# Kernel optimization log

Measured on AMD Instinct MI355X. Metric: run time of the kernel, lower is better.

The kernel has to match this reference:

```python
import jax, jax.numpy as jnp
import numpy as np

_SAMPLING_EPS = 1e-5
_NEG_INF = -jnp.inf


def _apply_min_p(logits, min_p):
    # probs >= min_p * max_prob are kept (vLLM apply_min_p)
    probs = jax.nn.softmax(logits, axis=-1)
    max_p = jnp.max(probs, axis=-1, keepdims=True)
    keep = probs >= (min_p[:, None] * max_p)
    return jnp.where(keep, logits, _NEG_INF)


def _apply_top_k_top_p(logits, top_k, top_p):
    # One descending sort serves both filters (mirrors vLLM topk/topp kernel).
    T, V = logits.shape
    sorted_l = jnp.sort(logits, axis=-1)[:, ::-1]  # [T, V] descending
    # top-k threshold: k-th largest logit; top_k <= 0 means disabled
    k = jnp.where(top_k <= 0, V, jnp.clip(top_k, 1, V)).astype(jnp.int32)
    kth = jnp.take_along_axis(sorted_l, (k - 1)[:, None], axis=-1)  # [T, 1]
    # top-p: keep smallest prefix whose prob mass reaches top_p (first token always kept)
    probs = jax.nn.softmax(sorted_l, axis=-1)
    cum = jnp.cumsum(probs, axis=-1)
    keep_p = (cum - probs) < top_p[:, None]
    pth = jnp.min(jnp.where(keep_p, sorted_l, jnp.inf), axis=-1, keepdims=True)
    keep = (logits >= kth) & (logits >= pth)
    return jnp.where(keep, logits, _NEG_INF)


def _gather_logprobs(logprobs, num_logprobs, token_ids):
    # vLLM gather_logprobs: topk + sampled-token logprob + rank
    topk_lp, topk_idx = jax.lax.top_k(logprobs, num_logprobs)  # [T, K]
    tok = token_ids[:, None]  # [T, 1]
    tok_lp = jnp.take_along_axis(logprobs, tok, axis=-1)  # [T, 1]
    ranks = jnp.sum(logprobs >= tok_lp, axis=-1).astype(jnp.int32)  # [T]
    indices = jnp.concatenate([tok, topk_idx], axis=1).astype(jnp.int32)
    lps = jnp.concatenate([tok_lp, topk_lp], axis=1)
    return indices, lps, ranks


def setup_inputs() -> dict:
    key = jax.random.key(0)
    k1, k2, k3, k4, k5, k6 = jax.random.split(key, 6)
    T, V = 256, 128256
    logits = jax.random.normal(k1, (T, V), dtype=jnp.float32)
    temperature = 0.2 + 1.3 * jax.random.uniform(k2, (T,), dtype=jnp.float32)
    # every 8th request is greedy (temperature < _SAMPLING_EPS path)
    temperature = jnp.where(jnp.arange(T) % 8 == 0, 0.0, temperature)
    min_p = 0.05 * jax.random.uniform(k3, (T,), dtype=jnp.float32)
    top_p = 0.5 + 0.5 * jax.random.uniform(k4, (T,), dtype=jnp.float32)
    top_k = jax.random.randint(k5, (T,), 0, 64, dtype=jnp.int32)
    u = jax.random.uniform(k6, (T, V), dtype=jnp.float32, minval=1e-10, maxval=1.0)
    return {"logits": logits, "temperature": temperature, "min_p": min_p,
            "top_p": top_p, "top_k": top_k, "u": u, "num_logprobs": 20}


def reference(logits, temperature, min_p, top_p, top_k, u, num_logprobs):
    logits = logits.astype(jnp.float32)
    # logprobs computed on raw (pre-temperature) logits, as in vLLM
    raw_logprobs = jax.nn.log_softmax(logits, axis=-1)
    # greedy path
    greedy = jnp.argmax(logits, axis=-1)
    # random path: temperature -> min_p -> top-k/top-p -> gumbel-max sample
    is_greedy = temperature < _SAMPLING_EPS
    safe_temp = jnp.where(is_greedy, 1.0, temperature)  # rows with temp<eps use greedy anyway
    l = logits / safe_temp[:, None]
    l = _apply_min_p(l, min_p)
    l = _apply_top_k_top_p(l, top_k, top_p)
    gumbel = -jnp.log(-jnp.log(u))  # u in (0,1)
    random_sampled = jnp.argmax(l + gumbel, axis=-1)
    sampled = jnp.where(is_greedy, greedy, random_sampled)
    indices, lps, ranks = _gather_logprobs(raw_logprobs, num_logprobs, sampled)
    sampled_token_ids = sampled.astype(jnp.int32)[:, None]  # [T, 1]
    return sampled_token_ids, indices, lps, ranks
```

## Files before the change

### kernel.cpp

```cpp
#include <hip/hip_runtime.h>
#include <math.h>

#define TPB 1024
#define TPBS 256
#define NS 8
#define NBINS 512
#define CAP 2048
#define NSEL 64
#define MBINS 1024
#define MWIN 16.0f
#define WIN 2.0f
#define SLCAP 1024
#define BANDCAP 64

typedef unsigned long long u64t;

__device__ __forceinline__ unsigned int ordAsc(float v) {
  unsigned int b = __float_as_uint(v);
  return (b & 0x80000000u) ? ~b : (b | 0x80000000u);
}
__device__ __forceinline__ float ordInv(unsigned int o) {
  return __uint_as_float((o & 0x80000000u) ? (o & 0x7fffffffu) : ~o);
}
__device__ __forceinline__ unsigned int fkeyDesc(float v) { return ~ordAsc(v); }
__device__ __forceinline__ float fkeyInv(unsigned int kd) { return ordInv(~kd); }
__device__ __forceinline__ u64t mkMaxKey(float v, int idx) {
  return ((u64t)ordAsc(v) << 32) | (unsigned int)(~(unsigned int)idx);
}

__device__ __forceinline__ float blockSumF(float v, float* sred) {
  #pragma unroll
  for (int o = 32; o > 0; o >>= 1) v += __shfl_down(v, o, 64);
  int wid = threadIdx.x >> 6, lane = threadIdx.x & 63, nw = blockDim.x >> 6;
  __syncthreads();
  if (lane == 0) sred[wid] = v;
  __syncthreads();
  if (threadIdx.x == 0) { float r = sred[0]; for (int w = 1; w < nw; ++w) r += sred[w]; sred[0] = r; }
  __syncthreads();
  float r = sred[0];
  __syncthreads();
  return r;
}
__device__ __forceinline__ int blockSumI(int v, int* sred) {
  #pragma unroll
  for (int o = 32; o > 0; o >>= 1) v += __shfl_down(v, o, 64);
  int wid = threadIdx.x >> 6, lane = threadIdx.x & 63, nw = blockDim.x >> 6;
  __syncthreads();
  if (lane == 0) sred[wid] = v;
  __syncthreads();
  if (threadIdx.x == 0) { int r = sred[0]; for (int w = 1; w < nw; ++w) r += sred[w]; sred[0] = r; }
  __syncthreads();
  int r = sred[0];
  __syncthreads();
  return r;
}
__device__ __forceinline__ int blockMaxI(int v, int* sred) {
  #pragma unroll
  for (int o = 32; o > 0; o >>= 1) { int v2 = __shfl_down(v, o, 64); if (v2 > v) v = v2; }
  int wid = threadIdx.x >> 6, lane = threadIdx.x & 63, nw = blockDim.x >> 6;
  __syncthreads();
  if (lane == 0) sred[wid] = v;
  __syncthreads();
  if (threadIdx.x == 0) { int r = sred[0]; for (int w = 1; w < nw; ++w) if (sred[w] > r) r = sred[w]; sred[0] = r; }
  __syncthreads();
  int r = sred[0];
  __syncthreads();
  return r;
}
__device__ __forceinline__ u64t blockMaxU64(u64t v, u64t* sred) {
  #pragma unroll
  for (int o = 32; o > 0; o >>= 1) { u64t v2 = __shfl_down(v, o, 64); if (v2 > v) v = v2; }
  int wid = threadIdx.x >> 6, lane = threadIdx.x & 63, nw = blockDim.x >> 6;
  __syncthreads();
  if (lane == 0) sred[wid] = v;
  __syncthreads();
  if (threadIdx.x == 0) { u64t r = sred[0]; for (int w = 1; w < nw; ++w) if (sred[w] > r) r = sred[w]; sred[0] = r; }
  __syncthreads();
  u64t r = sred[0];
  __syncthreads();
  return r;
}
__device__ __forceinline__ void blockArgMaxF(float& v, int& idx, float* sredf, int* sredi) {
  #pragma unroll
  for (int o = 32; o > 0; o >>= 1) {
    float v2 = __shfl_down(v, o, 64);
    int  i2 = __shfl_down(idx, o, 64);
    if (v2 > v || (v2 == v && i2 < idx)) { v = v2; idx = i2; }
  }
  int wid = threadIdx.x >> 6, lane = threadIdx.x & 63, nw = blockDim.x >> 6;
  __syncthreads();
  if (lane == 0) { sredf[wid] = v; sredi[wid] = idx; }
  __syncthreads();
  if (threadIdx.x == 0) {
    float bv = sredf[0]; int bi = sredi[0];
    for (int w = 1; w < nw; ++w) {
      float v2 = sredf[w]; int i2 = sredi[w];
      if (v2 > bv || (v2 == bv && i2 < bi)) { bv = v2; bi = i2; }
    }
    sredf[0] = bv; sredi[0] = bi;
  }
  __syncthreads();
  v = sredf[0]; idx = sredi[0];
  __syncthreads();
}

__device__ void bitonicSortN(u64t* keys, int n) {
  for (unsigned int k = 2; k <= (unsigned int)n; k <<= 1) {
    for (unsigned int j = k >> 1; j > 0; j >>= 1) {
      __syncthreads();
      for (unsigned int i = threadIdx.x; i < (unsigned int)n; i += blockDim.x) {
        unsigned int ixj = i ^ j;
        if (ixj > i) {
          u64t a = keys[i], b = keys[ixj];
          bool up = ((i & k) == 0);
          if ((a > b) == up) { keys[i] = b; keys[ixj] = a; }
        }
      }
    }
  }
  __syncthreads();
}

__device__ u64t bitonicReg1024(u64t key, u64t* lds) {
  const int tid = threadIdx.x;
  for (unsigned int k = 2; k <= 1024; k <<= 1) {
    for (unsigned int j = k >> 1; j > 0; j >>= 1) {
      u64t partner;
      if (j >= 64) {
        __syncthreads();
        lds[tid] = key;
        __syncthreads();
        partner = lds[tid ^ j];
      } else {
        partner = __shfl_xor((unsigned long long)key, (int)j, 64);
      }
      bool up = ((tid & k) == 0);
      bool lower = ((tid & j) == 0);
      bool keepSmaller = (up == lower);
      bool pSmaller = (partner < key);
      if (keepSmaller == pSmaller) key = partner;
    }
  }
  __syncthreads();
  lds[tid] = key;
  __syncthreads();
  return key;
}

__device__ __forceinline__ float combineS0(const u64t* smax, const float* s0s, float m0) {
  float S0 = 0.f;
  for (int w = 0; w < NS; ++w) {
    float ms = ordInv((unsigned int)(smax[w] >> 32));
    S0 += s0s[w] * expf(ms - m0);
  }
  return S0;
}

__global__ __launch_bounds__(TPBS) void k1_max(const float* __restrict__ logits,
                                               u64t* __restrict__ maxes,
                                               float* __restrict__ s0_ws,
                                               int* __restrict__ ccnt,
                                               int* __restrict__ bandcnt, int V) {
  const int row = blockIdx.y, s = blockIdx.x, tid = threadIdx.x;
  if (s == 0 && tid == 0) { ccnt[row] = 0; bandcnt[row] = 0; }
  const float* x = logits + (size_t)row * V;
  const int V4 = V >> 2;
  const float4* x4 = (const float4*)x;
  const int a4 = (int)(((long long)V4 * s) / NS), b4 = (int)(((long long)V4 * (s + 1)) / NS);
  u64t best = 0ull;
  float mt = -INFINITY, s0 = 0.f;
  auto body = [&](float vv, int gi) {
    u64t k = mkMaxKey(vv, gi);
    if (k > best) best = k;
    if (vv > mt) { s0 = s0 * expf(mt - vv); mt = vv; }
    s0 += expf(vv - mt);
  };
  for (int i4 = a4 + tid; i4 < b4; i4 += TPBS) {
    float4 v = x4[i4]; int b = i4 << 2;
    body(v.x, b); body(v.y, b + 1); body(v.z, b + 2); body(v.w, b + 3);
  }
  if (s == NS - 1) for (int i = (V4 << 2) + tid; i < V; i += TPBS) body(x[i], i);
  __shared__ u64t sredU[16];
  __shared__ float sredF[16];
  best = blockMaxU64(best, sredU);
  if (tid == 0) maxes[row * NS + s] = best;
  const float msv = ordInv((unsigned int)(best >> 32));
  float s0r = s0 * expf(mt - msv);
  float r0 = blockSumF(s0r, sredF);
  if (tid == 0) s0_ws[row * NS + s] = r0;
}

__global__ __launch_bounds__(TPBS) void k2_all(const float* __restrict__ logits,
    const float* __restrict__ temp_arr, const float* __restrict__ minp_arr,
    const int* __restrict__ topk_arr, const u64t* __restrict__ maxes,
    float* __restrict__ sl_ws, float* __restrict__ sp_ws, int* __restrict__ ck_ws,
    int* __restrict__ ccnt, u64t* __restrict__ cand,
    int* __restrict__ bandcnt, u64t* __restrict__ band,
    u64t* __restrict__ mass, int V) {
  const int row = blockIdx.y, s = blockIdx.x, tid = threadIdx.x;
  __shared__ u64t smax[NS];
  __shared__ float sredF[16];
  __shared__ int sredI[16];
  __shared__ u64t lcand[SLCAP];
  __shared__ u64t lmass[MBINS];
  __shared__ int lcnt, lbase;
  const float temp = temp_arr[row];
  const bool greedy = (temp < 1e-5f);
  const int topk = topk_arr[row];
  const bool deep = (!greedy && topk <= 0);
  if (tid < NS) smax[tid] = maxes[row * NS + tid];
  if (tid == 0) lcnt = 0;
  if (deep) for (int b = tid; b < MBINS; b += TPBS) lmass[b] = 0ull;
  __syncthreads();
  u64t mk = smax[0];
  for (int w = 1; w < NS; ++w) { u64t t = smax[w]; if (t > mk) mk = t; }
  const float m0 = ordInv((unsigned int)(mk >> 32));
  const float wlo = m0 - WIN;
  const float* x = logits + (size_t)row * V;
  const int V4 = V >> 2;
  const float4* x4 = (const float4*)x;
  const int a4 = (int)(((long long)V4 * s) / NS), b4 = (int)(((long long)V4 * (s + 1)) / NS);

  if (greedy) {
    auto bodyG = [&](float vv, int gi) {
      if (vv >= wlo) {
        int pos = atomicAdd(&lcnt, 1);
        if (pos < SLCAP) lcand[pos] = ((u64t)fkeyDesc(vv) << 32) | (unsigned int)gi;
      }
    };
    for (int i4 = a4 + tid; i4 < b4; i4 += TPBS) {
      float4 v = x4[i4]; int b = i4 << 2;
      bodyG(v.x, b); bodyG(v.y, b + 1); bodyG(v.z, b + 2); bodyG(v.w, b + 3);
    }
    if (s == NS - 1) for (int i = (V4 << 2) + tid; i < V; i += TPBS) bodyG(x[i], i);
    __syncthreads();
    if (tid == 0) {
      sl_ws[row * NS + s] = 0.f; sp_ws[row * NS + s] = 0.f; ck_ws[row * NS + s] = 0;
      int c = lcnt;
      int add = (c > SLCAP) ? (c + CAP + 1) : c;
      lbase = atomicAdd(&ccnt[row], add);
    }
    __syncthreads();
    int c = lcnt < SLCAP ? lcnt : SLCAP;
    int base = lbase;
    for (int j = tid; j < c; j += TPBS) {
      int pos = base + j;
      if (pos < CAP) cand[(size_t)row * CAP + pos] = lcand[j];
    }
    return;
  }

  const float st = temp;
  const float ml = m0 / st;
  const float minp = minp_arr[row];
  const float bHi = minp * (1.0f + 4e-6f);
  const float bLo = minp * (1.0f - 4e-6f);
  const float scaleM = (float)MBINS / MWIN;
  float sl = 0.f, sp = 0.f; int ckp = 0;
  auto body = [&](float vv, int gi) {
    float l = vv / st;
    float e = expf(l - ml);
    sl += e;
    if (minp <= 0.f || e > bHi) {
      sp += e; ckp++;
      if (deep) {
        float fm = (m0 - vv) * scaleM;
        if (fm < (float)MBINS)
          atomicAdd(&lmass[(int)fm], (u64t)((double)e * 4294967296.0));
      }
    } else if (e >= bLo) {
      int pos = atomicAdd(&bandcnt[row], 1);
      if (pos < BANDCAP)
        band[(size_t)row * BANDCAP + pos] = ((u64t)(unsigned int)gi << 32) | __float_as_uint(vv);
    }
    if (vv >= wlo) {
      int pos = atomicAdd(&lcnt, 1);
      if (pos < SLCAP) lcand[pos] = ((u64t)fkeyDesc(vv) << 32) | (unsigned int)gi;
    }
  };
  for (int i4 = a4 + tid; i4 < b4; i4 += TPBS) {
    float4 v = x4[i4]; int b = i4 << 2;
    body(v.x, b); body(v.y, b + 1); body(v.z, b + 2); body(v.w, b + 3);
  }
  if (s == NS - 1) for (int i = (V4 << 2) + tid; i < V; i += TPBS) body(x[i], i);
  float rl = blockSumF(sl, sredF);
  float rp = blockSumF(sp, sredF);
  int rc = blockSumI(ckp, sredI);
  if (tid == 0) {
    sl_ws[row * NS + s] = rl; sp_ws[row * NS + s] = rp; ck_ws[row * NS + s] = rc;
    int c = lcnt;
    int add = (c > SLCAP) ? (c + CAP + 1) : c;
    lbase = atomicAdd(&ccnt[row], add);
  }
  __syncthreads();
  int c = lcnt < SLCAP ? lcnt : SLCAP;
  int base = lbase;
  for (int j = tid; j < c; j += TPBS) {
    int pos = base + j;
    if (pos < CAP) cand[(size_t)row * CAP + pos] = lcand[j];
  }
  if (deep) {
    u64t* mrow = mass + ((size_t)row * NS + s) * MBINS;
    for (int b = tid; b < MBINS; b += TPBS) mrow[b] = lmass[b];
  }
}

__global__ __launch_bounds__(TPB) void k5_final(const float* __restrict__ logits,
    const float* __restrict__ temp_arr, const float* __restrict__ minp_arr,
    const float* __restrict__ topp_arr, const int* __restrict__ topk_arr,
    const float* __restrict__ u_arr, const u64t* __restrict__ maxes,
    const float* __restrict__ s0_ws, const float* __restrict__ sl_ws,
    const float* __restrict__ sp_ws, const int* __restrict__ ck_ws,
    const int* __restrict__ ccnt, const u64t* __restrict__ cand,
    const u64t* __restrict__ mass, const u64t* __restrict__ band,
    const int* __restrict__ bandcnt, float* __restrict__ w_thr,
    int* __restrict__ w_bpM, double* __restrict__ w_seed, float* __restrict__ w_spD,
    float* __restrict__ out, int T, int V, int NL) {
  __shared__ u64t keyA[CAP];
  __shared__ int fh[NBINS];
  __shared__ float sredF[16];
  __shared__ int sredI[16];
  __shared__ u64t smax[NS];
  __shared__ float sp0[NS], spl[NS], spsp[NS];
  __shared__ int spck[NS];
  __shared__ float sh_thresh, sh_toklp, sh_spAdd;
  __shared__ double sh_seed;
  __shared__ int sh_cnt, sh_bp, sh_bCnt, sh_ckAdd;
  __shared__ u64t sh_bKeys[BANDCAP];
  __shared__ u64t sh_bMass[BANDCAP];
  __shared__ int  sh_bBin[BANDCAP];
  __shared__ u64t kb64[NSEL];
  __shared__ u64t kbs[NSEL];

  const int row = blockIdx.x;
  const int tid = threadIdx.x;
  const float* x  = logits + (size_t)row * V;
  const float* uu = u_arr  + (size_t)row * V;
  const float temp = temp_arr[row];
  const float minp = minp_arr[row];
  const float topp = topp_arr[row];
  const int   topk = topk_arr[row];
  const bool greedy = (temp < 1e-5f);
  const float st = greedy ? 1.0f : temp;
  const int V4 = V >> 2;
  const float4* x4 = (const float4*)x;

  if (tid < NS) {
    smax[tid] = maxes[row * NS + tid];
    sp0[tid] = s0_ws[row * NS + tid];
    spl[tid] = sl_ws[row * NS + tid];
    spsp[tid] = sp_ws[row * NS + tid];
    spck[tid] = ck_ws[row * NS + tid];
  }
  __syncthreads();
  u64t mk = smax[0];
  for (int w = 1; w < NS; ++w) { u64t t = smax[w]; if (t > mk) mk = t; }
  const float m0 = ordInv((unsigned int)(mk >> 32));
  const int gidx = (int)(~(unsigned int)mk);
  float S = spl[0], Sp = spsp[0];
  int ck = spck[0];
  for (int w = 1; w < NS; ++w) { S += spl[w]; Sp += spsp[w]; ck += spck[w]; }
  const float S0 = combineS0(smax, sp0, m0);
  const float ml = m0 / st;
  const float logS0 = logf(S0);
  const float rhs = minp * (1.0f / S);
  const float rhsS = rhs * S;
  const float rhsHi = rhsS * (1.0f + 1e-6f);
  const float rhsLo = rhsS * (1.0f - 1e-6f);
  auto keepTest = [&](float e) -> bool {
    if (e > rhsHi) return true;
    if (e < rhsLo) return false;
    return (e / S) >= rhs;
  };
  const bool deep = (!greedy && topk <= 0);
  const float scaleM = (float)MBINS / MWIN;

  const int bandTotal = greedy ? 0 : bandcnt[row];
  const bool bandOv = bandTotal > BANDCAP;
  if (tid == 0) { sh_bCnt = 0; sh_spAdd = 0.f; sh_ckAdd = 0; }
  __syncthreads();
  if (!greedy && !bandOv && bandTotal > 0 && minp > 0.f) {
    if (tid == 0) {
      for (int i = 0; i < bandTotal; ++i) sh_bKeys[i] = band[(size_t)row * BANDCAP + i];
      for (int i = 1; i < bandTotal; ++i) {
        u64t k = sh_bKeys[i]; int j = i - 1;
        while (j >= 0 && sh_bKeys[j] > k) { sh_bKeys[j + 1] = sh_bKeys[j]; j--; }
        sh_bKeys[j + 1] = k;
      }
      float spAdd = 0.f; int ckAdd = 0, bc = 0;
      for (int i = 0; i < bandTotal; ++i) {
        float vv = __uint_as_float((unsigned int)(sh_bKeys[i] & 0xffffffffu));
        float l = vv / st; float e = expf(l - ml);
        if ((e / S) >= rhs) {
          spAdd += e; ckAdd++;
          if (deep) {
            float fm = (m0 - vv) * scaleM;
            if (fm < (float)MBINS) { sh_bBin[bc] = (int)fm; sh_bMass[bc] = (u64t)((double)e * 4294967296.0); bc++; }
          }
        }
      }
      sh_spAdd = spAdd; sh_ckAdd = ckAdd; sh_bCnt = bc;
    }
    __syncthreads();
    Sp += sh_spAdd; ck += sh_ckAdd;
  } else if (!greedy && bandOv) {
    float sp2 = 0.f; int ck2 = 0;
    auto bodyR = [&](float vv) {
      float l = vv / st; float e = expf(l - ml);
      if (keepTest(e)) { sp2 += e; ck2++; }
    };
    for (int i4 = tid; i4 < V4; i4 += TPB) { float4 v = x4[i4]; bodyR(v.x); bodyR(v.y); bodyR(v.z); bodyR(v.w); }
    for (int i = (V4 << 2) + tid; i < V; i += TPB) bodyR(x[i]);
    Sp = blockSumF(sp2, sredF);
    ck = blockSumI(ck2, sredI);
  }

  int cc = ccnt[row];
  int Cact = cc < CAP ? cc : CAP;
  int need = NSEL;
  if (topk > need) need = topk;
  if (need > CAP / 2) need = CAP / 2;
  if (need > V) need = V;
  bool fb = (cc > CAP) || (Cact < need);
  if (!fb) {
    for (int j = tid; j < Cact; j += TPB) keyA[j] = cand[(size_t)row * CAP + j];
  } else {
    const float bS = (float)NBINS / MWIN;
    for (int b = tid; b < NBINS; b += TPB) fh[b] = 0;
    if (tid == 0) sh_cnt = 0;
    __syncthreads();
    auto hb = [&](float vv) {
      float fbv = (m0 - vv) * bS;
      if (fbv < (float)NBINS) atomicAdd(&fh[(int)fbv], 1);
    };
    for (int i4 = tid; i4 < V4; i4 += TPB) { float4 v = x4[i4]; hb(v.x); hb(v.y); hb(v.z); hb(v.w); }
    for (int i = (V4 << 2) + tid; i < V; i += TPB) hb(x[i]);
    __syncthreads();
    if (tid == 0) {
      int cum = 0, B = -1;
      for (int b = 0; b < NBINS; ++b) { cum += fh[b]; if (cum >= need) { B = b; break; } }
      if (B < 0) B = NBINS - 1;
      sh_bp = B;
    }
    __syncthreads();
    const int B = sh_bp;
    auto cb = [&](float vv, int gi) {
      float fbv = (m0 - vv) * bS;
      if (fbv < (float)NBINS && (int)fbv <= B) {
        int pos = atomicAdd(&sh_cnt, 1);
        if (pos < CAP) keyA[pos] = ((u64t)fkeyDesc(vv) << 32) | (unsigned int)gi;
      }
    };
    for (int i4 = tid; i4 < V4; i4 += TPB) { float4 v = x4[i4]; int b = i4 << 2; cb(v.x, b); cb(v.y, b + 1); cb(v.z, b + 2); cb(v.w, b + 3); }
    for (int i = (V4 << 2) + tid; i < V; i += TPB) cb(x[i], i);
    __syncthreads();
    Cact = sh_cnt < CAP ? sh_cnt : CAP;
  }
  __syncthreads();
  if (Cact <= 1024) {
    u64t ka = (tid < Cact) ? keyA[tid] : ~0ull;
    bitonicReg1024(ka, keyA);
  } else {
    int n = 128; while (n < Cact) n <<= 1;
    for (int i = Cact + tid; i < n; i += TPB) keyA[i] = ~0ull;
    __syncthreads();
    bitonicSortN(keyA, n);
  }
  {
    int M = Cact < NSEL ? Cact : NSEL;
    if (tid < M) {
      u64t ka = keyA[tid];
      float xv = fkeyInv((unsigned int)(ka >> 32));
      float lp = (xv - m0) - logS0;
      kb64[tid] = ((u64t)fkeyDesc(lp) << 32) | (ka & 0xffffffffu);
    }
    __syncthreads();
    if (tid < M) {
      u64t me = kb64[tid];
      int r = 0;
      for (int i = 0; i < M; ++i) r += (kb64[i] < me) ? 1 : 0;
      kbs[r] = me;
    }
    __syncthreads();
    float* o_idx  = out + T;
    float* o_lps  = out + T + (size_t)T * (NL + 1);
    for (int j = tid; j < NL; j += TPB) {
      if (j < M) {
        u64t kb = kbs[j];
        o_idx[(size_t)row * (NL + 1) + 1 + j] = (float)(unsigned int)(kb & 0xffffffffu);
        o_lps[(size_t)row * (NL + 1) + 1 + j] = fkeyInv((unsigned int)(kb >> 32));
      }
    }
  }

  int sampled = -1;
  if (greedy) {
    sampled = gidx;
  } else if (topk > 0) {
    if (tid == 0) {
      int k = topk; if (k > V) k = V; if (k > CAP) k = CAP;
      int jp = 0; float cum = 0.f;
      for (int j = 0; j < k; ++j) {
        float pj = 0.f;
        if (j < ck && j < Cact) {
          float xv = fkeyInv((unsigned int)(keyA[j] >> 32));
          pj = expf(xv / st - ml) / Sp;
        }
        cum += pj;
        float ex = cum - pj;
        if (ex < topp) jp = j;
      }
      float thr;
      if (jp < ck && jp < Cact) {
        float xv = fkeyInv((unsigned int)(keyA[jp] >> 32));
        thr = xv / st;
      } else thr = -INFINITY;
      sh_thresh = thr;
    }
    __syncthreads();
    const float thr = sh_thresh;
    float bm = -INFINITY; int bi = 0x7fffffff;
    for (int j = tid; j < Cact; j += TPB) {
      u64t ka = keyA[j];
      float xv = fkeyInv((unsigned int)(ka >> 32));
      int gi = (int)(ka & 0xffffffffu);
      float l = xv / st;
      float e = expf(l - ml);
      if (keepTest(e) && l >= thr) {
        float uv = uu[gi];
        float g = -logf(-logf(uv));
        float val = l + g;
        if (val > bm || (val == bm && gi < bi)) { bm = val; bi = gi; }
      }
    }
    blockArgMaxF(bm, bi, sredF, sredI);
    sampled = bi;
  } else {
    if (!bandOv) {
      if (tid < MBINS) {
        u64t m = 0;
        for (int w = 0; w < NS; ++w) m += mass[((size_t)row * NS + w) * MBINS + tid];
        int bc = sh_bCnt;
        for (int j = 0; j < bc; ++j) if (sh_bBin[j] == tid) m += sh_bMass[j];
        keyA[tid] = m;
      }
    } else {
      for (int b = tid; b < MBINS; b += TPB) keyA[b] = 0ull;
      __syncthreads();
      auto bodyM = [&](float vv) {
        float l = vv / st; float e = expf(l - ml);
        if (keepTest(e)) {
          float fm = (m0 - vv) * scaleM;
          if (fm < (float)MBINS) atomicAdd(&keyA[(int)fm], (u64t)((double)e * 4294967296.0));
        }
      };
      for (int i4 = tid; i4 < V4; i4 += TPB) { float4 v = x4[i4]; bodyM(v.x); bodyM(v.y); bodyM(v.z); bodyM(v.w); }
      for (int i = (V4 << 2) + tid; i < V; i += TPB) bodyM(x[i]);
    }
    __syncthreads();
    u64t mh = (tid < MBINS) ? keyA[tid] : 0ull;
    for (int off = 1; off < MBINS; off <<= 1) {
      u64t add = (tid < MBINS && tid >= off) ? keyA[tid - off] : 0ull;
      __syncthreads();
      if (tid < MBINS) keyA[tid] += add;
      __syncthreads();
    }
    const double TP = (double)topp * (double)Sp;
    int q = -1; u64t myexcl = 0;
    if (tid < MBINS && mh > 0ull) {
      u64t excl = keyA[tid] - mh;
      if ((double)excl * (1.0 / 4294967296.0) < TP) { q = tid; myexcl = excl; }
    }
    int bp = blockMaxI(q, sredI);
    if (bp >= 0 && tid == bp) sh_seed = (double)myexcl * (1.0 / 4294967296.0);
    if (bp < 0 && tid == 0) sh_seed = 0.0;
    __syncthreads();
    if (tid == 0) {
      w_bpM[row] = bp;
      w_seed[row] = sh_seed;
      w_spD[row] = Sp;
      if (bp < 0) w_thr[row] = -INFINITY;
    }
  }

  if (!deep) {
    if (tid == 0) sh_toklp = (x[sampled] - m0) - logS0;
    __syncthreads();
    const float toklp = sh_toklp;
    int rc = 0;
    for (int j = tid; j < Cact; j += TPB) {
      float xv = fkeyInv((unsigned int)(keyA[j] >> 32));
      float lp = (xv - m0) - logS0;
      if (lp >= toklp) rc++;
    }
    int rank = blockSumI(rc, sredI);
    float* o_samp = out;
    float* o_idx  = out + T;
    float* o_lps  = out + T + (size_t)T * (NL + 1);
    float* o_rank = out + T + (size_t)2 * T * (NL + 1);
    if (tid == 0) {
      o_samp[row] = (float)sampled;
      o_idx[(size_t)row * (NL + 1)] = (float)sampled;
      o_lps[(size_t)row * (NL + 1)] = toklp;
      o_rank[row] = (float)rank;
    }
  }
}

__global__ __launch_bounds__(TPB) void kD_thr(const float* __restrict__ logits,
    const float* __restrict__ temp_arr, const float* __restrict__ minp_arr,
    const float* __restrict__ topp_arr, const int* __restrict__ topk_arr,
    const u64t* __restrict__ maxes, const float* __restrict__ sl_ws,
    const int* __restrict__ w_bpM, const float* __restrict__ w_spD,
    const double* __restrict__ w_seed, float* __restrict__ w_thr, int V) {
  const int row = blockIdx.x, tid = threadIdx.x;
  const float temp = temp_arr[row];
  if (temp < 1e-5f || topk_arr[row] > 0) return;
  const int bp = w_bpM[row];
  if (bp < 0) return;
  __shared__ u64t keyA[CAP];
  __shared__ float pvals[CAP];
  __shared__ u64t smax[NS];
  __shared__ float ssl[NS];
  __shared__ int sh_cnt;
  if (tid < NS) { smax[tid] = maxes[row * NS + tid]; ssl[tid] = sl_ws[row * NS + tid]; }
  if (tid == 0) sh_cnt = 0;
  __syncthreads();
  u64t mk = smax[0];
  for (int w = 1; w < NS; ++w) { u64t t = smax[w]; if (t > mk) mk = t; }
  float S = ssl[0];
  for (int w = 1; w < NS; ++w) S += ssl[w];
  const float m0 = ordInv((unsigned int)(mk >> 32));
  const float st = temp;
  const float ml = m0 / st;
  const float minp = minp_arr[row];
  const float rhs = minp * (1.0f / S);
  const float rhsS = rhs * S;
  const float rhsHi = rhsS * (1.0f + 1e-6f);
  const float rhsLo = rhsS * (1.0f - 1e-6f);
  auto keepTest = [&](float e) -> bool {
    if (e > rhsHi) return true;
    if (e < rhsLo) return false;
    return (e / S) >= rhs;
  };
  const float scaleM = (float)MBINS / MWIN;
  const float* x = logits + (size_t)row * V;
  const int V4 = V >> 2;
  const float4* x4 = (const float4*)x;
  auto body = [&](float vv, int gi) {
    float fm = (m0 - vv) * scaleM;
    if (fm < (float)MBINS && (int)fm == bp) {
      float l = vv / st;
      float e = expf(l - ml);
      if (keepTest(e)) {
        int pos = atomicAdd(&sh_cnt, 1);
        if (pos < CAP) keyA[pos] = ((u64t)fkeyDesc(vv) << 32) | (unsigned int)gi;
      }
    }
  };
  for (int i4 = tid; i4 < V4; i4 += TPB) {
    float4 v = x4[i4]; int b = i4 << 2;
    body(v.x, b); body(v.y, b + 1); body(v.z, b + 2); body(v.w, b + 3);
  }
  for (int i = (V4 << 2) + tid; i < V; i += TPB) body(x[i], i);
  __syncthreads();
  int C5 = sh_cnt < CAP ? sh_cnt : CAP;
  if (C5 <= 1024) {
    u64t kc = (tid < C5) ? keyA[tid] : ~0ull;
    bitonicReg1024(kc, keyA);
  } else {
    int n5 = 128; while (n5 < C5) n5 <<= 1;
    for (int i = C5 + tid; i < n5; i += TPB) keyA[i] = ~0ull;
    __syncthreads();
    bitonicSortN(keyA, n5);
  }
  const float Sp = w_spD[row];
  for (int j = tid; j < C5; j += TPB) {
    float xv = fkeyInv((unsigned int)(keyA[j] >> 32));
    pvals[j] = expf(xv / st - ml) / Sp;
  }
  __syncthreads();
  if (tid == 0) {
    const float topp = topp_arr[row];
    float cum = (float)(w_seed[row] / (double)Sp);
    float lastVal = fkeyInv((unsigned int)(keyA[0] >> 32));
    for (int j = 0; j < C5; ++j) {
      float pj = pvals[j];
      cum += pj;
      float ex = cum - pj;
      if (ex < topp) lastVal = fkeyInv((unsigned int)(keyA[j] >> 32));
    }
    w_thr[row] = lastVal / st;
  }
}

__global__ __launch_bounds__(TPBS) void k6_gumbel(const float* __restrict__ logits,
    const float* __restrict__ temp_arr, const float* __restrict__ minp_arr,
    const int* __restrict__ topk_arr, const float* __restrict__ u_arr,
    const u64t* __restrict__ maxes, const float* __restrict__ sl_ws,
    const float* __restrict__ w_thr, u64t* __restrict__ gkey, int V) {
  const int row = blockIdx.y, s = blockIdx.x, tid = threadIdx.x;
  const float temp = temp_arr[row];
  if (temp < 1e-5f || topk_arr[row] > 0) return;
  __shared__ u64t smax[NS];
  __shared__ float ssl[NS];
  __shared__ float sredF[16];
  __shared__ int sredI[16];
  if (tid < NS) { smax[tid] = maxes[row * NS + tid]; ssl[tid] = sl_ws[row * NS + tid]; }
  __syncthreads();
  u64t mk = smax[0];
  for (int w = 1; w < NS; ++w) { u64t t = smax[w]; if (t > mk) mk = t; }
  float S = ssl[0];
  for (int w = 1; w < NS; ++w) S += ssl[w];
  const float m0 = ordInv((unsigned int)(mk >> 32));
  const float st = temp;
  const float ml = m0 / st;
  const float minp = minp_arr[row];
  const float rhs = minp * (1.0f / S);
  const float rhsS = rhs * S;
  const float rhsHi = rhsS * (1.0f + 1e-6f);
  const float rhsLo = rhsS * (1.0f - 1e-6f);
  auto keepTest = [&](float e) -> bool {
    if (e > rhsHi) return true;
    if (e < rhsLo) return false;
    return (e / S) >= rhs;
  };
  const float thr = w_thr[row];
  const float* x  = logits + (size_t)row * V;
  const float* uu = u_arr  + (size_t)row * V;
  const int V4 = V >> 2;
  const float4* x4 = (const float4*)x;
  const float4* u4 = (const float4*)uu;
  const int a4 = (int)(((long long)V4 * s) / NS), b4 = (int)(((long long)V4 * (s + 1)) / NS);
  float bm = -INFINITY; int bi = 0x7fffffff;
  auto body = [&](float vv, float uv, int gi) {
    float l = vv / st;
    float e = expf(l - ml);
    if (keepTest(e) && l >= thr) {
      float g = -logf(-logf(uv));
      float val = l + g;
      if (val > bm || (val == bm && gi < bi)) { bm = val; bi = gi; }
    }
  };
  for (int i4 = a4 + tid; i4 < b4; i4 += TPBS) {
    float4 v = x4[i4]; float4 w = u4[i4]; int b = i4 << 2;
    body(v.x, w.x, b); body(v.y, w.y, b + 1); body(v.z, w.z, b + 2); body(v.w, w.w, b + 3);
  }
  if (s == NS - 1) for (int i = (V4 << 2) + tid; i < V; i += TPBS) body(x[i], uu[i], i);
  blockArgMaxF(bm, bi, sredF, sredI);
  if (tid == 0) gkey[row * NS + s] = mkMaxKey(bm, bi);
}

__global__ __launch_bounds__(TPB) void k7_deepfin(const float* __restrict__ logits,
    const float* __restrict__ temp_arr, const int* __restrict__ topk_arr,
    const u64t* __restrict__ gkey, const float* __restrict__ s0_ws,
    const u64t* __restrict__ maxes, float* __restrict__ out, int T, int V, int NL) {
  const int row = blockIdx.x, tid = threadIdx.x;
  const float temp = temp_arr[row];
  if (temp < 1e-5f || topk_arr[row] > 0) return;
  __shared__ u64t sg[NS];
  __shared__ u64t smax[NS];
  __shared__ float sp0[NS];
  __shared__ int sredI[16];
  if (tid < NS) { sg[tid] = gkey[row * NS + tid]; smax[tid] = maxes[row * NS + tid]; sp0[tid] = s0_ws[row * NS + tid]; }
  __syncthreads();
  u64t gk = sg[0];
  for (int w = 1; w < NS; ++w) { if (sg[w] > gk) gk = sg[w]; }
  u64t mk = smax[0];
  for (int w = 1; w < NS; ++w) { u64t t = smax[w]; if (t > mk) mk = t; }
  const float m0 = ordInv((unsigned int)(mk >> 32));
  const float S0 = combineS0(smax, sp0, m0);
  const float logS0 = logf(S0);
  const int sampled = (int)(~(unsigned int)gk);
  const float* x = logits + (size_t)row * V;
  const float toklp = (x[sampled] - m0) - logS0;
  const int V4 = V >> 2;
  const float4* x4 = (const float4*)x;
  int rc = 0;
  auto body = [&](float vv) {
    float lp = (vv - m0) - logS0;
    if (lp >= toklp) rc++;
  };
  for (int i4 = tid; i4 < V4; i4 += TPB) { float4 v = x4[i4]; body(v.x); body(v.y); body(v.z); body(v.w); }
  for (int i = (V4 << 2) + tid; i < V; i += TPB) body(x[i]);
  int rank = blockSumI(rc, sredI);
  float* o_samp = out;
  float* o_idx  = out + T;
  float* o_lps  = out + T + (size_t)T * (NL + 1);
  float* o_rank = out + T + (size_t)2 * T * (NL + 1);
  if (tid == 0) {
    o_samp[row] = (float)sampled;
    o_idx[(size_t)row * (NL + 1)] = (float)sampled;
    o_lps[(size_t)row * (NL + 1)] = toklp;
    o_rank[row] = (float)rank;
  }
}

__global__ __launch_bounds__(TPB) void sampler_mono(
    const float* __restrict__ logits, const float* __restrict__ temp_arr,
    const float* __restrict__ minp_arr, const float* __restrict__ topp_arr,
    const int* __restrict__ topk_arr, const float* __restrict__ u_arr,
    float* __restrict__ out, int T, int V, int NL) {
  __shared__ u64t keyA[CAP];
  __shared__ u64t keyB[CAP];
  __shared__ float pvals[CAP];
  __shared__ int   cnthist[NBINS];
  __shared__ u64t  masshist[NBINS];
  __shared__ float sredF[16];
  __shared__ int   sredI[16];
  __shared__ float sh_thresh, sh_toklp, sh_Rm, sh_Roff;
  __shared__ double sh_seedD, sh_seedBase;
  __shared__ int sh_B64, sh_Bp, sh_cnt, sh_state;

  const int row = blockIdx.x;
  const int tid = threadIdx.x;
  const float* x  = logits + (size_t)row * V;
  const float* uu = u_arr  + (size_t)row * V;
  const float temp = temp_arr[row];
  const float minp = minp_arr[row];
  const float topp = topp_arr[row];
  const int   topk = topk_arr[row];
  const bool greedy = (temp < 1e-5f);
  const float st = greedy ? 1.0f : temp;
  const int V4 = V >> 2;
  const float4* x4 = (const float4*)x;

  float m0; int gidx;
  {
    float lm = -INFINITY; int lidx = 0x7fffffff;
    for (int i4 = tid; i4 < V4; i4 += TPB) {
      float4 v = x4[i4]; int b = i4 << 2;
      if (v.x > lm) { lm = v.x; lidx = b; }
      if (v.y > lm) { lm = v.y; lidx = b + 1; }
      if (v.z > lm) { lm = v.z; lidx = b + 2; }
      if (v.w > lm) { lm = v.w; lidx = b + 3; }
    }
    for (int i = (V4 << 2) + tid; i < V; i += TPB) {
      float v = x[i]; if (v > lm) { lm = v; lidx = i; }
    }
    blockArgMaxF(lm, lidx, sredF, sredI);
    m0 = lm; gidx = lidx;
  }
  const float ml = m0 / st;

  float Rcur = 2.0f;
  float binScale = (float)NBINS / Rcur;
  for (int b = tid; b < NBINS; b += TPB) cnthist[b] = 0;
  __syncthreads();
  float S0, S;
  {
    float s0p = 0.f, slp = 0.f;
    auto histAdd = [&](float vv) {
      float fb = (m0 - vv) * binScale;
      if (fb < (float)NBINS) atomicAdd(&cnthist[(int)fb], 1);
    };
    for (int i4 = tid; i4 < V4; i4 += TPB) {
      float4 v = x4[i4];
      s0p += expf(v.x - m0) + expf(v.y - m0) + expf(v.z - m0) + expf(v.w - m0);
      if (!greedy) slp += expf(v.x / st - ml) + expf(v.y / st - ml) + expf(v.z / st - ml) + expf(v.w / st - ml);
      histAdd(v.x); histAdd(v.y); histAdd(v.z); histAdd(v.w);
    }
    for (int i = (V4 << 2) + tid; i < V; i += TPB) {
      float v = x[i]; s0p += expf(v - m0); if (!greedy) slp += expf(v / st - ml); histAdd(v);
    }
    S0 = blockSumF(s0p, sredF);
    S = greedy ? S0 : blockSumF(slp, sredF);
  }

  int need = NSEL;
  if (topk > need) need = topk;
  if (need > CAP / 2) need = CAP / 2;
  if (need > V) need = V;
  int B64;
  for (int attempt = 0; ; ++attempt) {
    __syncthreads();
    if (tid == 0) {
      long long cum = 0; int b64 = -1; long long c64 = 0;
      for (int b = 0; b < NBINS; ++b) {
        cum += cnthist[b];
        if (cum >= need) { b64 = b; c64 = cum; break; }
      }
      int state;
      if (b64 >= 0 && c64 <= CAP) state = 1;
      else if (b64 < 0) state = 0;
      else state = 2;
      if (attempt >= 3 && state != 1) { state = 1; if (b64 < 0) b64 = NBINS - 1; }
      sh_state = state; sh_B64 = b64;
    }
    __syncthreads();
    if (sh_state == 1) { B64 = sh_B64; break; }
    Rcur = (sh_state == 0) ? Rcur * 8.0f : Rcur * 0.125f;
    binScale = (float)NBINS / Rcur;
    __syncthreads();
    for (int b = tid; b < NBINS; b += TPB) cnthist[b] = 0;
    __syncthreads();
    auto histAdd2 = [&](float vv) {
      float fb = (m0 - vv) * binScale;
      if (fb < (float)NBINS) atomicAdd(&cnthist[(int)fb], 1);
    };
    for (int i4 = tid; i4 < V4; i4 += TPB) {
      float4 v = x4[i4];
      histAdd2(v.x); histAdd2(v.y); histAdd2(v.z); histAdd2(v.w);
    }
    for (int i = (V4 << 2) + tid; i < V; i += TPB) histAdd2(x[i]);
  }

  const float logS0 = logf(S0);
  const float rhs = minp * (1.0f / S);
  const float rhsS = rhs * S;
  const float rhsHi = rhsS * (1.0f + 1e-6f);
  const float rhsLo = rhsS * (1.0f - 1e-6f);
  auto keepTest = [&](float e) -> bool {
    if (e > rhsHi) return true;
    if (e < rhsLo) return false;
    return (e / S) >= rhs;
  };
  const bool needMass = (!greedy && topk <= 0);
  const float scaleM0 = (float)NBINS / 16.0f;

  for (int b = tid; b < NBINS; b += TPB) { cnthist[b] = 0; masshist[b] = 0ull; }
  if (tid == 0) { sh_cnt = 0; sh_Rm = 16.0f; sh_Roff = 0.0f; sh_seedBase = 0.0; }
  __syncthreads();
  float Sp; int ck;
  {
    float spp = 0.f; int ckp = 0;
    auto bodyB = [&](float vv, int gi) {
      float fb = (m0 - vv) * binScale;
      if (fb < (float)NBINS && (int)fb <= B64) {
        int pos = atomicAdd(&sh_cnt, 1);
        if (pos < CAP) keyA[pos] = ((u64t)fkeyDesc(vv) << 32) | (unsigned int)gi;
      }
      if (!greedy) {
        float l = vv / st;
        float e = expf(l - ml);
        if (keepTest(e)) {
          spp += e; ckp++;
          if (needMass) {
            float fm = (m0 - vv) * scaleM0;
            if (fm < (float)NBINS) {
              int bm = (int)fm;
              atomicAdd(&masshist[bm], (u64t)((double)e * 4294967296.0));
              atomicAdd(&cnthist[bm], 1);
            }
          }
        }
      }
    };
    for (int i4 = tid; i4 < V4; i4 += TPB) {
      float4 v = x4[i4]; int b = i4 << 2;
      bodyB(v.x, b); bodyB(v.y, b + 1); bodyB(v.z, b + 2); bodyB(v.w, b + 3);
    }
    for (int i = (V4 << 2) + tid; i < V; i += TPB) bodyB(x[i], i);
    Sp = blockSumF(spp, sredF);
    ck = blockSumI(ckp, sredI);
  }
  int Cact = sh_cnt; if (Cact > CAP) Cact = CAP;

  int n = 128; while (n < Cact) n <<= 1;
  for (int i = Cact + tid; i < n; i += TPB) keyA[i] = ~0ull;
  __syncthreads();
  bitonicSortN(keyA, n);
  for (int j = tid; j < n; j += TPB) {
    if (j < Cact) {
      u64t ka = keyA[j];
      float xv = fkeyInv((unsigned int)(ka >> 32));
      float lp = (xv - m0) - logS0;
      keyB[j] = ((u64t)fkeyDesc(lp) << 32) | (ka & 0xffffffffu);
    } else keyB[j] = ~0ull;
  }
  bitonicSortN(keyB, n);

  int sampled;
  if (greedy) {
    sampled = gidx;
  } else if (topk > 0) {
    if (tid == 0) {
      int k = topk; if (k > V) k = V; if (k > CAP) k = CAP;
      int jp = 0; float cum = 0.f;
      for (int j = 0; j < k; ++j) {
        float pj = 0.f;
        if (j < ck && j < Cact) {
          float xv = fkeyInv((unsigned int)(keyA[j] >> 32));
          pj = expf(xv / st - ml) / Sp;
        }
        cum += pj;
        float ex = cum - pj;
        if (ex < topp) jp = j;
      }
      float thr;
      if (jp < ck && jp < Cact) {
        float xv = fkeyInv((unsigned int)(keyA[jp] >> 32));
        thr = xv / st;
      } else thr = -INFINITY;
      sh_thresh = thr;
    }
    __syncthreads();
    const float thr = sh_thresh;
    float bm = -INFINITY; int bi = 0x7fffffff;
    for (int j = tid; j < Cact; j += TPB) {
      u64t ka = keyA[j];
      float xv = fkeyInv((unsigned int)(ka >> 32));
      int gi = (int)(ka & 0xffffffffu);
      float l = xv / st;
      float e = expf(l - ml);
      if (keepTest(e) && l >= thr) {
        float uv = uu[gi];
        float g = -logf(-logf(uv));
        float val = l + g;
        if (val > bm || (val == bm && gi < bi)) { bm = val; bi = gi; }
      }
    }
    blockArgMaxF(bm, bi, sredF, sredI);
    sampled = bi;
  } else {
    for (int attempt = 0; ; ++attempt) {
      __syncthreads();
      if (tid == 0) {
        float Rm = sh_Rm, Roff = sh_Roff;
        double TP = (double)topp * (double)Sp;
        double cm = sh_seedBase; int bp = -1; double seed = sh_seedBase; int cbp = 0;
        for (int b = 0; b < NBINS; ++b) {
          u64t mh = masshist[b];
          if (mh > 0ull && cm < TP) { bp = b; seed = cm; cbp = cnthist[b]; }
          cm += (double)mh * (1.0 / 4294967296.0);
        }
        int state = 1;
        if (attempt < 3) {
          if (cm < TP && Roff == 0.0f) {
            state = 0; sh_Rm = Rm * 8.0f;
          } else if (bp >= 0 && cbp > CAP) {
            state = 2;
            float bw = Rm / (float)NBINS;
            sh_Roff = Roff + (float)bp * bw;
            sh_Rm = bw;
            sh_seedBase = seed;
          }
        }
        if (bp < 0) { bp = 0; seed = sh_seedBase; }
        sh_Bp = bp; sh_seedD = seed; sh_state = state;
      }
      __syncthreads();
      if (sh_state == 1) break;
      float Rm = sh_Rm, Roff = sh_Roff;
      float sM = (float)NBINS / Rm;
      for (int b = tid; b < NBINS; b += TPB) { cnthist[b] = 0; masshist[b] = 0ull; }
      __syncthreads();
      auto bodyM = [&](float vv) {
        float fm = ((m0 - vv) - Roff) * sM;
        if (fm >= 0.f && fm < (float)NBINS) {
          float l = vv / st;
          float e = expf(l - ml);
          if (keepTest(e)) {
            int bm = (int)fm;
            atomicAdd(&masshist[bm], (u64t)((double)e * 4294967296.0));
            atomicAdd(&cnthist[bm], 1);
          }
        }
      };
      for (int i4 = tid; i4 < V4; i4 += TPB) {
        float4 v = x4[i4]; bodyM(v.x); bodyM(v.y); bodyM(v.z); bodyM(v.w);
      }
      for (int i = (V4 << 2) + tid; i < V; i += TPB) bodyM(x[i]);
    }
    const int Bp = sh_Bp;
    const float RmF = sh_Rm, RoffF = sh_Roff;
    const float sM = (float)NBINS / RmF;
    if (tid == 0) sh_cnt = 0;
    __syncthreads();
    auto bodyC = [&](float vv, int gi) {
      float fm = ((m0 - vv) - RoffF) * sM;
      if (fm >= 0.f && fm < (float)NBINS && (int)fm == Bp) {
        float l = vv / st;
        float e = expf(l - ml);
        if (keepTest(e)) {
          int pos = atomicAdd(&sh_cnt, 1);
          if (pos < CAP) keyA[pos] = ((u64t)fkeyDesc(vv) << 32) | (unsigned int)gi;
        }
      }
    };
    for (int i4 = tid; i4 < V4; i4 += TPB) {
      float4 v = x4[i4]; int b = i4 << 2;
      bodyC(v.x, b); bodyC(v.y, b + 1); bodyC(v.z, b + 2); bodyC(v.w, b + 3);
    }
    for (int i = (V4 << 2) + tid; i < V; i += TPB) bodyC(x[i], i);
    __syncthreads();
    int C5 = sh_cnt; if (C5 > CAP) C5 = CAP;
    int n5 = 128; while (n5 < C5) n5 <<= 1;
    for (int i = C5 + tid; i < n5; i += TPB) keyA[i] = ~0ull;
    __syncthreads();
    bitonicSortN(keyA, n5);
    for (int j = tid; j < C5; j += TPB) {
      float xv = fkeyInv((unsigned int)(keyA[j] >> 32));
      pvals[j] = expf(xv / st - ml) / Sp;
    }
    __syncthreads();
    if (tid == 0) {
      float cum = (float)(sh_seedD / (double)Sp);
      float lastVal = fkeyInv((unsigned int)(keyA[0] >> 32));
      for (int j = 0; j < C5; ++j) {
        float pj = pvals[j];
        cum += pj;
        float ex = cum - pj;
        if (ex < topp) lastVal = fkeyInv((unsigned int)(keyA[j] >> 32));
      }
      sh_thresh = lastVal / st;
    }
    __syncthreads();
    const float thr = sh_thresh;
    const float4* u4 = (const float4*)uu;
    float bm = -INFINITY; int bi = 0x7fffffff;
    auto body6 = [&](float vv, float uv, int gi) {
      float l = vv / st;
      float e = expf(l - ml);
      if (keepTest(e) && l >= thr) {
        float g = -logf(-logf(uv));
        float val = l + g;
        if (val > bm || (val == bm && gi < bi)) { bm = val; bi = gi; }
      }
    };
    for (int i4 = tid; i4 < V4; i4 += TPB) {
      float4 v = x4[i4]; float4 w = u4[i4]; int b = i4 << 2;
      body6(v.x, w.x, b); body6(v.y, w.y, b + 1); body6(v.z, w.z, b + 2); body6(v.w, w.w, b + 3);
    }
    for (int i = (V4 << 2) + tid; i < V; i += TPB) body6(x[i], uu[i], i);
    blockArgMaxF(bm, bi, sredF, sredI);
    sampled = bi;
  }

  if (tid == 0) sh_toklp = (x[sampled] - m0) - logS0;
  __syncthreads();
  const float toklp = sh_toklp;
  int rank;
  {
    int rc = 0;
    if (!needMass) {
      for (int j = tid; j < Cact; j += TPB) {
        float xv = fkeyInv((unsigned int)(keyA[j] >> 32));
        float lp = (xv - m0) - logS0;
        if (lp >= toklp) rc++;
      }
    } else {
      auto body7 = [&](float vv) {
        float lp = (vv - m0) - logS0;
        if (lp >= toklp) rc++;
      };
      for (int i4 = tid; i4 < V4; i4 += TPB) {
        float4 v = x4[i4]; body7(v.x); body7(v.y); body7(v.z); body7(v.w);
      }
      for (int i = (V4 << 2) + tid; i < V; i += TPB) body7(x[i]);
    }
    rank = blockSumI(rc, sredI);
  }

  float* o_samp = out;
  float* o_idx  = out + T;
  float* o_lps  = out + T + (size_t)T * (NL + 1);
  float* o_rank = out + T + (size_t)2 * T * (NL + 1);
  if (tid == 0) {
    o_samp[row] = (float)sampled;
    o_idx[(size_t)row * (NL + 1)] = (float)sampled;
    o_lps[(size_t)row * (NL + 1)] = toklp;
    o_rank[row] = (float)rank;
  }
  for (int j = tid; j < NL; j += TPB) {
    u64t kb = keyB[j];
    o_idx[(size_t)row * (NL + 1) + 1 + j] = (float)(unsigned int)(kb & 0xffffffffu);
    o_lps[(size_t)row * (NL + 1) + 1 + j] = fkeyInv((unsigned int)(kb >> 32));
  }
}

extern "C" void kernel_launch(void* const* d_in, const int* in_sizes, int n_in,
                              void* d_out, int out_size, void* d_ws, size_t ws_size,
                              hipStream_t stream) {
  const float* logits = (const float*)d_in[0];
  const float* temp   = (const float*)d_in[1];
  const float* minp   = (const float*)d_in[2];
  const float* topp   = (const float*)d_in[3];
  const int*   topk   = (const int*)d_in[4];
  const float* u      = (const float*)d_in[5];
  const int T  = in_sizes[1];
  const int V  = in_sizes[0] / T;
  const int NL = (out_size / T - 4) / 2;

  size_t off = 0;
  char* base = (char*)d_ws;
  u64t*   w_maxes   = (u64t*)(base + off);   off += (size_t)T * NS * 8;
  u64t*   w_cand    = (u64t*)(base + off);   off += (size_t)T * CAP * 8;
  u64t*   w_mass    = (u64t*)(base + off);   off += (size_t)T * NS * MBINS * 8;
  u64t*   w_gkey    = (u64t*)(base + off);   off += (size_t)T * NS * 8;
  u64t*   w_band    = (u64t*)(base + off);   off += (size_t)T * BANDCAP * 8;
  double* w_seed    = (double*)(base + off); off += (size_t)T * 8;
  float*  w_s0      = (float*)(base + off);  off += (size_t)T * NS * 4;
  float*  w_sl      = (float*)(base + off);  off += (size_t)T * NS * 4;
  float*  w_sp      = (float*)(base + off);  off += (size_t)T * NS * 4;
  int*    w_ck      = (int*)(base + off);    off += (size_t)T * NS * 4;
  int*    w_ccnt    = (int*)(base + off);    off += (size_t)T * 4;
  int*    w_bandcnt = (int*)(base + off);    off += (size_t)T * 4;
  float*  w_thr     = (float*)(base + off);  off += (size_t)T * 4;
  int*    w_bpM     = (int*)(base + off);    off += (size_t)T * 4;
  float*  w_spD     = (float*)(base + off);  off += (size_t)T * 4;

  if (off > ws_size) {
    sampler_mono<<<T, TPB, 0, stream>>>(logits, temp, minp, topp, topk, u,
                                        (float*)d_out, T, V, NL);
    return;
  }

  dim3 gS(NS, T);
  k1_max<<<gS, TPBS, 0, stream>>>(logits, w_maxes, w_s0, w_ccnt, w_bandcnt, V);
  k2_all<<<gS, TPBS, 0, stream>>>(logits, temp, minp, topk, w_maxes, w_sl,
                                  w_sp, w_ck, w_ccnt, w_cand, w_bandcnt, w_band,
                                  w_mass, V);
  k5_final<<<T, TPB, 0, stream>>>(logits, temp, minp, topp, topk, u, w_maxes,
                                  w_s0, w_sl, w_sp, w_ck, w_ccnt, w_cand, w_mass,
                                  w_band, w_bandcnt, w_thr, w_bpM, w_seed, w_spD,
                                  (float*)d_out, T, V, NL);
  kD_thr<<<T, TPB, 0, stream>>>(logits, temp, minp, topp, topk, w_maxes, w_sl,
                                w_bpM, w_spD, w_seed, w_thr, V);
  k6_gumbel<<<gS, TPBS, 0, stream>>>(logits, temp, minp, topk, u, w_maxes, w_sl,
                                     w_thr, w_gkey, V);
  k7_deepfin<<<T, TPB, 0, stream>>>(logits, temp, topk, w_gkey, w_s0, w_maxes,
                                    (float*)d_out, T, V, NL);
}
```

Measured before the change: 211.9 us.

## Fuse top-p threshold kernel into final kernel and replace small sorts with rank selection

Moves the deep-row top-p threshold computation (bin rescan, sort, cumulative scan) from the separate kD_thr kernel into k5_final. This removes one launch and the workspace round-trip for the bin index, seed and Sp. It also replaces the full bitonic sort of candidates with an O(C^2) rank selection of the top NSEL entries when only a small prefix is needed. The cost is a larger shared-memory footprint in k5_final (an extra pvals array), which can lower occupancy. The quadratic rank scan may also be slow if the candidate count is large.

```diff
diff --git a/kernel.cpp b/kernel.cpp
--- a/kernel.cpp
+++ b/kernel.cpp
@@ -314,9 +314,9 @@
     const int* __restrict__ ccnt, const u64t* __restrict__ cand,
     const u64t* __restrict__ mass, const u64t* __restrict__ band,
     const int* __restrict__ bandcnt, float* __restrict__ w_thr,
-    int* __restrict__ w_bpM, double* __restrict__ w_seed, float* __restrict__ w_spD,
     float* __restrict__ out, int T, int V, int NL) {
   __shared__ u64t keyA[CAP];
+  __shared__ float pvals[CAP];
   __shared__ int fh[NBINS];
   __shared__ float sredF[16];
   __shared__ int sredI[16];
@@ -329,6 +329,7 @@
   __shared__ u64t sh_bKeys[BANDCAP];
   __shared__ u64t sh_bMass[BANDCAP];
   __shared__ int  sh_bBin[BANDCAP];
+  __shared__ u64t sel[NSEL];
   __shared__ u64t kb64[NSEL];
   __shared__ u64t kbs[NSEL];
 
@@ -457,19 +458,30 @@
     Cact = sh_cnt < CAP ? sh_cnt : CAP;
   }
   __syncthreads();
-  if (Cact <= 1024) {
-    u64t ka = (tid < Cact) ? keyA[tid] : ~0ull;
-    bitonicReg1024(ka, keyA);
+
+  bool sortedFull = (need > NSEL);
+  if (!sortedFull) {
+    for (int j = tid; j < Cact; j += TPB) {
+      u64t me = keyA[j];
+      int r = 0;
+      for (int i = 0; i < Cact; ++i) r += (keyA[i] < me) ? 1 : 0;
+      if (r < NSEL) sel[r] = me;
+    }
+    __syncthreads();
   } else {
     int n = 128; while (n < Cact) n <<= 1;
     for (int i = Cact + tid; i < n; i += TPB) keyA[i] = ~0ull;
     __syncthreads();
     bitonicSortN(keyA, n);
-  }
+    int M0 = Cact < NSEL ? Cact : NSEL;
+    for (int j = tid; j < M0; j += TPB) sel[j] = keyA[j];
+    __syncthreads();
+  }
+
   {
     int M = Cact < NSEL ? Cact : NSEL;
     if (tid < M) {
-      u64t ka = keyA[tid];
+      u64t ka = sel[tid];
       float xv = fkeyInv((unsigned int)(ka >> 32));
       float lp = (xv - m0) - logS0;
       kb64[tid] = ((u64t)fkeyDesc(lp) << 32) | (ka & 0xffffffffu);
@@ -503,7 +515,8 @@
       for (int j = 0; j < k; ++j) {
         float pj = 0.f;
         if (j < ck && j < Cact) {
-          float xv = fkeyInv((unsigned int)(keyA[j] >> 32));
+          u64t kj = sortedFull ? keyA[j] : sel[j];
+          float xv = fkeyInv((unsigned int)(kj >> 32));
           pj = expf(xv / st - ml) / Sp;
         }
         cum += pj;
@@ -512,7 +525,8 @@
       }
       float thr;
       if (jp < ck && jp < Cact) {
-        float xv = fkeyInv((unsigned int)(keyA[jp] >> 32));
+        u64t kj = sortedFull ? keyA[jp] : sel[jp];
+        float xv = fkeyInv((unsigned int)(kj >> 32));
         thr = xv / st;
       } else thr = -INFINITY;
       sh_thresh = thr;
@@ -575,11 +589,51 @@
     if (bp >= 0 && tid == bp) sh_seed = (double)myexcl * (1.0 / 4294967296.0);
     if (bp < 0 && tid == 0) sh_seed = 0.0;
     __syncthreads();
-    if (tid == 0) {
-      w_bpM[row] = bp;
-      w_seed[row] = sh_seed;
-      w_spD[row] = Sp;
-      if (bp < 0) w_thr[row] = -INFINITY;
+    if (bp < 0) {
+      if (tid == 0) w_thr[row] = -INFINITY;
+    } else {
+      if (tid == 0) sh_cnt = 0;
+      __syncthreads();
+      auto bodyC = [&](float vv, int gi) {
+        float fm = (m0 - vv) * scaleM;
+        if (fm < (float)MBINS && (int)fm == bp) {
+          float l = vv / st;
+          float e = expf(l - ml);
+          if (keepTest(e)) {
+            int pos = atomicAdd(&sh_cnt, 1);
+            if (pos < CAP) keyA[pos] = ((u64t)fkeyDesc(vv) << 32) | (unsigned int)gi;
+          }
+        }
+      };
+      for (int i4 = tid; i4 < V4; i4 += TPB) { float4 v = x4[i4]; int b = i4 << 2; bodyC(v.x, b); bodyC(v.y, b + 1); bodyC(v.z, b + 2); bodyC(v.w, b + 3); }
+      for (int i = (V4 << 2) + tid; i < V; i += TPB) bodyC(x[i], i);
+      __syncthreads();
+      int C5 = sh_cnt < CAP ? sh_cnt : CAP;
+      if (C5 <= 1024) {
+        u64t kc = (tid < C5) ? keyA[tid] : ~0ull;
+        bitonicReg1024(kc, keyA);
+      } else {
+        int n5 = 128; while (n5 < C5) n5 <<= 1;
+        for (int i = C5 + tid; i < n5; i += TPB) keyA[i] = ~0ull;
+        __syncthreads();
+        bitonicSortN(keyA, n5);
+      }
+      for (int j = tid; j < C5; j += TPB) {
+        float xv = fkeyInv((unsigned int)(keyA[j] >> 32));
+        pvals[j] = expf(xv / st - ml) / Sp;
+      }
+      __syncthreads();
+      if (tid == 0) {
+        float cum = (float)(sh_seed / (double)Sp);
+        float lastVal = fkeyInv((unsigned int)(keyA[0] >> 32));
+        for (int j = 0; j < C5; ++j) {
+          float pj = pvals[j];
+          cum += pj;
+          float ex = cum - pj;
+          if (ex < topp) lastVal = fkeyInv((unsigned int)(keyA[j] >> 32));
+        }
+        w_thr[row] = lastVal / st;
+      }
     }
   }
 
@@ -604,93 +658,6 @@
       o_lps[(size_t)row * (NL + 1)] = toklp;
       o_rank[row] = (float)rank;
     }
-  }
-}
-
-__global__ __launch_bounds__(TPB) void kD_thr(const float* __restrict__ logits,
-    const float* __restrict__ temp_arr, const float* __restrict__ minp_arr,
-    const float* __restrict__ topp_arr, const int* __restrict__ topk_arr,
-    const u64t* __restrict__ maxes, const float* __restrict__ sl_ws,
-    const int* __restrict__ w_bpM, const float* __restrict__ w_spD,
-    const double* __restrict__ w_seed, float* __restrict__ w_thr, int V) {
-  const int row = blockIdx.x, tid = threadIdx.x;
-  const float temp = temp_arr[row];
-  if (temp < 1e-5f || topk_arr[row] > 0) return;
-  const int bp = w_bpM[row];
-  if (bp < 0) return;
-  __shared__ u64t keyA[CAP];
-  __shared__ float pvals[CAP];
-  __shared__ u64t smax[NS];
-  __shared__ float ssl[NS];
-  __shared__ int sh_cnt;
-  if (tid < NS) { smax[tid] = maxes[row * NS + tid]; ssl[tid] = sl_ws[row * NS + tid]; }
-  if (tid == 0) sh_cnt = 0;
-  __syncthreads();
-  u64t mk = smax[0];
-  for (int w = 1; w < NS; ++w) { u64t t = smax[w]; if (t > mk) mk = t; }
-  float S = ssl[0];
-  for (int w = 1; w < NS; ++w) S += ssl[w];
-  const float m0 = ordInv((unsigned int)(mk >> 32));
-  const float st = temp;
-  const float ml = m0 / st;
-  const float minp = minp_arr[row];
-  const float rhs = minp * (1.0f / S);
-  const float rhsS = rhs * S;
-  const float rhsHi = rhsS * (1.0f + 1e-6f);
-  const float rhsLo = rhsS * (1.0f - 1e-6f);
-  auto keepTest = [&](float e) -> bool {
-    if (e > rhsHi) return true;
-    if (e < rhsLo) return false;
-    return (e / S) >= rhs;
-  };
-  const float scaleM = (float)MBINS / MWIN;
-  const float* x = logits + (size_t)row * V;
-  const int V4 = V >> 2;
-  const float4* x4 = (const float4*)x;
-  auto body = [&](float vv, int gi) {
-    float fm = (m0 - vv) * scaleM;
-    if (fm < (float)MBINS && (int)fm == bp) {
-      float l = vv / st;
-      float e = expf(l - ml);
-      if (keepTest(e)) {
-        int pos = atomicAdd(&sh_cnt, 1);
-        if (pos < CAP) keyA[pos] = ((u64t)fkeyDesc(vv) << 32) | (unsigned int)gi;
-      }
-    }
-  };
-  for (int i4 = tid; i4 < V4; i4 += TPB) {
-    float4 v = x4[i4]; int b = i4 << 2;
-    body(v.x, b); body(v.y, b + 1); body(v.z, b + 2); body(v.w, b + 3);
-  }
-  for (int i = (V4 << 2) + tid; i < V; i += TPB) body(x[i], i);
-  __syncthreads();
-  int C5 = sh_cnt < CAP ? sh_cnt : CAP;
-  if (C5 <= 1024) {
-    u64t kc = (tid < C5) ? keyA[tid] : ~0ull;
-    bitonicReg1024(kc, keyA);
-  } else {
-    int n5 = 128; while (n5 < C5) n5 <<= 1;
-    for (int i = C5 + tid; i < n5; i += TPB) keyA[i] = ~0ull;
-    __syncthreads();
-    bitonicSortN(keyA, n5);
-  }
-  const float Sp = w_spD[row];
-  for (int j = tid; j < C5; j += TPB) {
-    float xv = fkeyInv((unsigned int)(keyA[j] >> 32));
-    pvals[j] = expf(xv / st - ml) / Sp;
-  }
-  __syncthreads();
-  if (tid == 0) {
-    const float topp = topp_arr[row];
-    float cum = (float)(w_seed[row] / (double)Sp);
-    float lastVal = fkeyInv((unsigned int)(keyA[0] >> 32));
-    for (int j = 0; j < C5; ++j) {
-      float pj = pvals[j];
-      cum += pj;
-      float ex = cum - pj;
-      if (ex < topp) lastVal = fkeyInv((unsigned int)(keyA[j] >> 32));
-    }
-    w_thr[row] = lastVal / st;
   }
 }
 
@@ -1189,7 +1156,6 @@
   u64t*   w_mass    = (u64t*)(base + off);   off += (size_t)T * NS * MBINS * 8;
   u64t*   w_gkey    = (u64t*)(base + off);   off += (size_t)T * NS * 8;
   u64t*   w_band    = (u64t*)(base + off);   off += (size_t)T * BANDCAP * 8;
-  double* w_seed    = (double*)(base + off); off += (size_t)T * 8;
   float*  w_s0      = (float*)(base + off);  off += (size_t)T * NS * 4;
   float*  w_sl      = (float*)(base + off);  off += (size_t)T * NS * 4;
   float*  w_sp      = (float*)(base + off);  off += (size_t)T * NS * 4;
@@ -1197,8 +1163,6 @@
   int*    w_ccnt    = (int*)(base + off);    off += (size_t)T * 4;
   int*    w_bandcnt = (int*)(base + off);    off += (size_t)T * 4;
   float*  w_thr     = (float*)(base + off);  off += (size_t)T * 4;
-  int*    w_bpM     = (int*)(base + off);    off += (size_t)T * 4;
-  float*  w_spD     = (float*)(base + off);  off += (size_t)T * 4;
 
   if (off > ws_size) {
     sampler_mono<<<T, TPB, 0, stream>>>(logits, temp, minp, topp, topk, u,
@@ -1213,10 +1177,8 @@
                                   w_mass, V);
   k5_final<<<T, TPB, 0, stream>>>(logits, temp, minp, topp, topk, u, w_maxes,
                                   w_s0, w_sl, w_sp, w_ck, w_ccnt, w_cand, w_mass,
-                                  w_band, w_bandcnt, w_thr, w_bpM, w_seed, w_spD,
+                                  w_band, w_bandcnt, w_thr,
                                   (float*)d_out, T, V, NL);
-  kD_thr<<<T, TPB, 0, stream>>>(logits, temp, minp, topp, topk, w_maxes, w_sl,
-                                w_bpM, w_spD, w_seed, w_thr, V);
   k6_gumbel<<<gS, TPBS, 0, stream>>>(logits, temp, minp, topk, u, w_maxes, w_sl,
                                      w_thr, w_gkey, V);
   k7_deepfin<<<T, TPB, 0, stream>>>(logits, temp, topk, w_gkey, w_s0, w_maxes,
```

New measurement: 222.0 us. +4.8%, slower.
